# Kernel optimization log

Hardware: AMD Instinct MI355X
Metric: run time of the kernel (lower is better)

The kernel has to match this reference:

```python
import jax, jax.numpy as jnp
import numpy as np

N_NODES = 100000
N_EDGES = 3200000
D = 256
L = 3
BN_EPS = 1e-5


def setup_inputs() -> dict:
    key = jax.random.key(0)
    ks = jax.random.split(key, 6)
    scale = 1.0 / np.sqrt(D)
    x = jax.random.normal(ks[0], (N_NODES, D), dtype=jnp.float32)
    W = jax.random.normal(ks[1], (L, D, D), dtype=jnp.float32) * scale
    b = jnp.zeros((L, D), dtype=jnp.float32)
    Wl = jax.random.normal(ks[2], (L, D, D), dtype=jnp.float32) * scale
    bl = jnp.zeros((L, D), dtype=jnp.float32)
    gamma = jnp.ones((L, D), dtype=jnp.float32)
    beta = jnp.zeros((L, D), dtype=jnp.float32)
    src = jax.random.randint(ks[3], (N_EDGES,), 0, N_NODES, dtype=jnp.int32)
    dst = jax.random.randint(ks[4], (N_EDGES,), 0, N_NODES, dtype=jnp.int32)
    return {"x": x, "W": W, "b": b, "Wl": Wl, "bl": bl,
            "gamma": gamma, "beta": beta, "src": src, "dst": dst}


def _gcn_head(x, W, b, Wl, bl, gamma, beta, src, dst):
    n = x.shape[0]
    ones = jnp.ones((src.shape[0],), dtype=x.dtype)
    # degrees (clamped to 1, as DGL GraphConv does)
    deg_out = jnp.maximum(jax.ops.segment_sum(ones, src, num_segments=n), 1.0)
    deg_in = jnp.maximum(jax.ops.segment_sum(ones, dst, num_segments=n), 1.0)
    inv_sqrt_out = (deg_out ** -0.5)[:, None]  # [N,1]
    inv_sqrt_in = (deg_in ** -0.5)[:, None]

    h = x
    for l in range(W.shape[0]):
        # GraphConv, norm='both': D_in^{-1/2} A D_out^{-1/2} h W + b
        hs = h * inv_sqrt_out
        agg = jax.ops.segment_sum(hs[src], dst, num_segments=n)  # [N,D]
        agg = agg * inv_sqrt_in
        out = agg @ W[l] + b[l]
        # residual + optional linear on the layer input
        out = out + h + (h @ Wl[l] + bl[l])
        # BatchNorm1d over nodes (training-style batch stats, biased var)
        mean = jnp.mean(out, axis=0)
        var = jnp.var(out, axis=0)
        out = gamma[l] * (out - mean) * jax.lax.rsqrt(var + BN_EPS) + beta[l]
        # ReLU (Dropout treated as identity / eval mode)
        h = jax.nn.relu(out)
    return h


def reference(x, W, b, Wl, bl, gamma, beta, src, dst):
    return _gcn_head(x, W, b, Wl, bl, gamma, beta, src, dst)
```

## Files before the change

kernel.cpp:

```cpp
#include <hip/hip_runtime.h>

#define D 256
#define BN_EPS 1e-5f

typedef __attribute__((ext_vector_type(8))) short short8;
typedef __attribute__((ext_vector_type(4))) float f32x4;
typedef __attribute__((ext_vector_type(2))) float f32x2;

__device__ __forceinline__ float b2f(ushort u) {
    union { unsigned u; float f; } c; c.u = ((unsigned)u) << 16; return c.f;
}
__device__ __forceinline__ ushort f2b(float f) {
    union { float f; unsigned u; } c; c.f = f;
    return (ushort)((c.u + 0x7fffu + ((c.u >> 16) & 1u)) >> 16);
}

typedef __attribute__((address_space(1))) const void gv_t;
typedef __attribute__((address_space(3))) void lv_t;
__device__ __forceinline__ void gld16(const void* g, void* l) {
    __builtin_amdgcn_global_load_lds((gv_t*)g, (lv_t*)l, 16, 0, 0);
}

__device__ __forceinline__ uint2 pk_fp8x8(const float* r) {
    unsigned w0 = 0, w1 = 0;
    w0 = __builtin_amdgcn_cvt_pk_fp8_f32(r[0], r[1], w0, false);
    w0 = __builtin_amdgcn_cvt_pk_fp8_f32(r[2], r[3], w0, true);
    w1 = __builtin_amdgcn_cvt_pk_fp8_f32(r[4], r[5], w1, false);
    w1 = __builtin_amdgcn_cvt_pk_fp8_f32(r[6], r[7], w1, true);
    return make_uint2(w0, w1);
}


#define HB 64

__global__ __launch_bounds__(256) void hist_kernel(const int* __restrict__ src,
                                                   const int* __restrict__ dst,
                                                   unsigned* __restrict__ P, int E) {
    __shared__ unsigned lhist[16384];
    int combo = blockIdx.y;
    const int* arr = (combo >> 2) ? dst : src;
    unsigned base = (unsigned)(combo & 3) << 15;
    for (int j = threadIdx.x; j < 16384; j += 256) lhist[j] = 0;
    __syncthreads();
    int i0 = (blockIdx.x * 256 + threadIdx.x) * 4;
    int stride = HB * 256 * 4;
    for (int i = i0; i < E; i += stride) {
        if (i + 3 < E) {
            int4 v = *(const int4*)(arr + i);
            unsigned r0 = (unsigned)v.x - base;
            unsigned r1 = (unsigned)v.y - base;
            unsigned r2 = (unsigned)v.z - base;
            unsigned r3 = (unsigned)v.w - base;
            if (r0 < 32768u) atomicAdd(&lhist[r0 >> 1], 1u << ((r0 & 1) << 4));
            if (r1 < 32768u) atomicAdd(&lhist[r1 >> 1], 1u << ((r1 & 1) << 4));
            if (r2 < 32768u) atomicAdd(&lhist[r2 >> 1], 1u << ((r2 & 1) << 4));
            if (r3 < 32768u) atomicAdd(&lhist[r3 >> 1], 1u << ((r3 & 1) << 4));
        } else {
            for (int j = i; j < E; j++) {
                unsigned r = (unsigned)arr[j] - base;
                if (r < 32768u) atomicAdd(&lhist[r >> 1], 1u << ((r & 1) << 4));
            }
        }
    }
    __syncthreads();
    unsigned* dstp = P + ((size_t)(combo * HB + blockIdx.x) << 14);
    for (int j = threadIdx.x; j < 16384; j += 256) dstp[j] = lhist[j];
}

__global__ void histreduce_kernel(const unsigned* __restrict__ P,
                                  int* __restrict__ cntO, int* __restrict__ cntI, int N) {
    int g = blockIdx.x * 256 + threadIdx.x;
    int array = g >> 16;
    int p = g & 65535;
    int range = p >> 14;
    int j = p & 16383;
    const unsigned* Pp = P + ((size_t)((array * 4 + range) * HB) << 14) + j;
    unsigned s = 0;
#pragma unroll 8
    for (int b = 0; b < HB; b++) s += Pp[(size_t)b << 14];
    int bin = (range << 15) + 2 * j;
    int* cnt = array ? cntI : cntO;
    if (bin < N)     cnt[bin]     = (int)(s & 0xFFFFu);
    if (bin + 1 < N) cnt[bin + 1] = (int)(s >> 16);
}

__global__ void invsqrt_kernel(const int* __restrict__ cntO, const int* __restrict__ cntI,
                               float* __restrict__ invO, float* __restrict__ invOI,
                               float* __restrict__ sqrtO, int N) {
    int i = blockIdx.x * blockDim.x + threadIdx.x;
    if (i < N) {
        float dO = (float)max(cntO[i], 1);
        float io = rsqrtf(dO);
        invO[i] = io;
        sqrtO[i] = sqrtf(dO);
        invOI[i] = io * rsqrtf((float)max(cntI[i], 1));
    }
}

__global__ void scan1_kernel(const int* __restrict__ cnt, int* __restrict__ off,
                             int* __restrict__ bsum, int n) {
    __shared__ int s[256];
    int t = threadIdx.x;
    int i0 = blockIdx.x * 1024 + t * 4;
    int v0 = (i0 < n) ? ((cnt[i0] + 7) & ~7) : 0;
    int v1 = (i0 + 1 < n) ? ((cnt[i0 + 1] + 7) & ~7) : 0;
    int v2 = (i0 + 2 < n) ? ((cnt[i0 + 2] + 7) & ~7) : 0;
    int v3 = (i0 + 3 < n) ? ((cnt[i0 + 3] + 7) & ~7) : 0;
    int tsum = v0 + v1 + v2 + v3;
    s[t] = tsum;
    __syncthreads();
    for (int d = 1; d < 256; d <<= 1) {
        int x = (t >= d) ? s[t - d] : 0;
        __syncthreads();
        s[t] += x;
        __syncthreads();
    }
    int excl = s[t] - tsum;
    if (i0 < n)     off[i0]     = excl;
    if (i0 + 1 < n) off[i0 + 1] = excl + v0;
    if (i0 + 2 < n) off[i0 + 2] = excl + v0 + v1;
    if (i0 + 3 < n) off[i0 + 3] = excl + v0 + v1 + v2;
    if (t == 255) bsum[blockIdx.x] = s[255];
}

__global__ void scan2_kernel(int* __restrict__ bsum, int nb) {
    __shared__ int s[256];
    int t = threadIdx.x;
    int v = (t < nb) ? bsum[t] : 0;
    s[t] = v;
    __syncthreads();
    for (int d = 1; d < 256; d <<= 1) {
        int x = (t >= d) ? s[t - d] : 0;
        __syncthreads();
        s[t] += x;
        __syncthreads();
    }
    if (t < nb) bsum[t] = s[t] - v;
    if (t == nb - 1) bsum[1023] = s[t];
}

__global__ void scan3_kernel(int* __restrict__ off, const int* __restrict__ bsum,
                             int* __restrict__ bucketCur, int n) {
    int i = blockIdx.x * blockDim.x + threadIdx.x;
    if (i < n) {
        int v = off[i] + bsum[i >> 10];
        off[i] = v;
        if ((i & 255) == 0) bucketCur[i >> 8] = v;
    } else if (i == n) {
        off[n] = bsum[1023];
    }
}


#define NBKMAX 512

__global__ __launch_bounds__(256) void partA_kernel(const int* __restrict__ src,
                                                    const int* __restrict__ dst,
                                                    int* __restrict__ bucketCur,
                                                    unsigned* __restrict__ pairs,
                                                    int E, int NBK) {
    __shared__ int cnt[NBKMAX];
    __shared__ int base_s[NBKMAX];
    for (int j = threadIdx.x; j < NBK; j += 256) cnt[j] = 0;
    __syncthreads();
    for (int i = blockIdx.x * 256 + threadIdx.x; i < E; i += gridDim.x * 256)
        atomicAdd(&cnt[((unsigned)dst[i]) >> 8], 1);
    __syncthreads();
    for (int j = threadIdx.x; j < NBK; j += 256) {
        base_s[j] = atomicAdd(&bucketCur[j], cnt[j]);
        cnt[j] = 0;
    }
    __syncthreads();
    for (int i = blockIdx.x * 256 + threadIdx.x; i < E; i += gridDim.x * 256) {
        unsigned d = (unsigned)dst[i];
        unsigned b = d >> 8;
        int pos = base_s[b] + atomicAdd(&cnt[b], 1);
        pairs[pos] = ((unsigned)src[i] << 8) | (d & 255u);
    }
}

#define BCAP 14336

__global__ __launch_bounds__(256) void partB_kernel(const unsigned* __restrict__ pairs,
                                                    const int* __restrict__ off,
                                                    const int* __restrict__ bucketCur,
                                                    int* __restrict__ srcS, int N) {
    __shared__ int curL[256];
    __shared__ int stage[BCAP];
    int b = blockIdx.x;
    int n0 = b << 8;
    int n1 = min(n0 + 256, N);
    int base = off[n0];
    int len = off[n1] - base;
    if (len > BCAP) len = BCAP;
    for (int j = threadIdx.x; j < len; j += 256) stage[j] = N;
    int nn = n1 - n0;
    for (int i = threadIdx.x; i < nn; i += 256) curL[i] = off[n0 + i] - base;
    __syncthreads();
    int cntB = bucketCur[b] - base;
    for (int j = threadIdx.x; j < cntB; j += 256) {
        unsigned p = pairs[base + j];
        int pos = atomicAdd(&curL[p & 255u], 1);
        if (pos < BCAP) stage[pos] = (int)(p >> 8);
    }
    __syncthreads();
    for (int j4 = threadIdx.x; j4 * 4 < len; j4 += 256)
        *(int4*)(srcS + base + j4 * 4) = *(const int4*)(stage + j4 * 4);
}

__global__ void init_pad_kernel(ushort* __restrict__ X, unsigned* __restrict__ X8,
                                int N, long strideH) {
    int t = threadIdx.x;
    X[(size_t)N * D + t] = 0;
    if (t < 64) X8[(t >> 5) * strideH + (size_t)N * 32 + (t & 31)] = 0;
}


__global__ void prep_w_kernel(const float* __restrict__ W, const float* __restrict__ Wl,
                              const float* __restrict__ b, const float* __restrict__ bl,
                              ushort* __restrict__ Wt, float* __restrict__ bcat, int L) {
    int idx = blockIdx.x * blockDim.x + threadIdx.x;
    int k = idx & 511;
    int n = (idx >> 9) & 255;
    int l = idx >> 17;
    if (l >= L) return;
    float v;
    if (k < 256) {
        v = W[(size_t)l * 65536 + k * 256 + n];
    } else {
        v = Wl[(size_t)l * 65536 + (k - 256) * 256 + n];
        if (k - 256 == n) v += 1.0f;
    }
    Wt[idx] = f2b(v);
    if (k == 0) bcat[l * 256 + n] = b[l * 256 + n] + bl[l * 256 + n];
}

__global__ void x2b_kernel(const float* __restrict__ x, const float* __restrict__ invO,
                           ushort* __restrict__ hs, unsigned* __restrict__ hs8,
                           long strideH, long n8) {
    long i8 = (long)blockIdx.x * blockDim.x + threadIdx.x;
    if (i8 >= n8) return;
    long row = i8 >> 5;
    float sc = invO[row];
    float4 a = ((const float4*)x)[i8 * 2];
    float4 b = ((const float4*)x)[i8 * 2 + 1];
    float r[8] = { a.x * sc, a.y * sc, a.z * sc, a.w * sc,
                   b.x * sc, b.y * sc, b.z * sc, b.w * sc };
    ushort v[8];
#pragma unroll
    for (int j = 0; j < 8; j++) v[j] = f2b(r[j]);
    *(short8*)(hs + i8 * 8) = *(short8*)v;
    long H = (i8 >> 4) & 1;
    *(uint2*)(hs8 + H * strideH + row * 32 + (i8 & 15) * 2) = pk_fp8x8(r);
}


__global__ void aggregate_kernel(const unsigned* __restrict__ X8,
                                 const float* __restrict__ invOI,
                                 const int* __restrict__ off, const int* __restrict__ srcS,
                                 ushort* __restrict__ aggs, long strideH, int N) {
    const unsigned* hs8h = X8 + blockIdx.y * strideH;
    ushort* aggsh = aggs + blockIdx.y * 128;
    int tid = threadIdx.x;
    int wid = tid >> 6, lane = tid & 63;
    int l32 = lane & 31;
    int node = blockIdx.x * 8 + wid * 2 + (lane >> 5);
    if (blockIdx.x * 8 + wid * 2 >= N) return;
    bool valid = node < N;
    int e0 = valid ? off[node] : 0;
    int e1 = valid ? off[node + 1] : 0;
    f32x2 A01 = {0.f, 0.f}, A23 = {0.f, 0.f};
    for (int e = e0; e < e1; e += 8) {
        int4 c0 = *(const int4*)(srcS + e);
        int4 c1 = *(const int4*)(srcS + e + 4);
        unsigned g0 = hs8h[(size_t)c0.x * 32 + l32];
        unsigned g1 = hs8h[(size_t)c0.y * 32 + l32];
        unsigned g2 = hs8h[(size_t)c0.z * 32 + l32];
        unsigned g3 = hs8h[(size_t)c0.w * 32 + l32];
        unsigned g4 = hs8h[(size_t)c1.x * 32 + l32];
        unsigned g5 = hs8h[(size_t)c1.y * 32 + l32];
        unsigned g6 = hs8h[(size_t)c1.z * 32 + l32];
        unsigned g7 = hs8h[(size_t)c1.w * 32 + l32];
#pragma unroll
        for (int q = 0; q < 8; q++) {
            unsigned g = (q == 0) ? g0 : (q == 1) ? g1 : (q == 2) ? g2 : (q == 3) ? g3
                       : (q == 4) ? g4 : (q == 5) ? g5 : (q == 6) ? g6 : g7;
            A01 += __builtin_amdgcn_cvt_pk_f32_fp8(g, false);
            A23 += __builtin_amdgcn_cvt_pk_f32_fp8(g, true);
        }
    }
    if (valid) {
        float wi = invOI[node];
        ushort4 o;
        o.x = f2b(A01[0] * wi); o.y = f2b(A01[1] * wi);
        o.z = f2b(A23[0] * wi); o.w = f2b(A23[1] * wi);
        *(ushort4*)(aggsh + (size_t)node * D + l32 * 4) = o;
    }
}


#define BSOFF 4096

__global__ __launch_bounds__(512, 4) void gemm_kernel(
        const ushort* __restrict__ aggs, const ushort* __restrict__ hs,
        const ushort* __restrict__ Wt,  const float* __restrict__ bcat,
        const float* __restrict__ sqrtO,
        ushort* __restrict__ tmp, float* __restrict__ bnsum, float* __restrict__ bnsq,
        int M) {
    __shared__ short SH[12288];

    int bm0 = blockIdx.x * 128;
    if (bm0 >= M) return;

    int tid = threadIdx.x;
    int wid = tid >> 6, lane = tid & 63;
    int wr = wid >> 2, wc = wid & 3;
    int lrow = lane & 15, lkh = lane >> 4;
    int srow = lane >> 2;
    int sseg = (lane & 3) ^ ((srow >> 1) & 3);

    f32x4 acc[4][4] = {};

#pragma unroll
    for (int k0 = 0; k0 < 512; k0 += 32) {
        {
            int kk_ = k0 & 255;
            const ushort* Ah_ = (k0 < 256) ? aggs : hs;
            gld16(Ah_ + (size_t)(bm0 + wid * 16 + srow) * 256 + kk_ + sseg * 8,
                  SH + (wid * 16) * 32);
            const ushort* gb_ = Wt + (size_t)(wid * 32 + srow) * 512 + k0 + sseg * 8;
            gld16(gb_,            SH + BSOFF + (wid * 32) * 32);
            gld16(gb_ + 16 * 512, SH + BSOFF + (wid * 32 + 16) * 32);
        }
        __syncthreads();

        short8 a[4], bfr[4];
#pragma unroll
        for (int m = 0; m < 4; m++) {
            int ra = wr * 64 + m * 16 + lrow;
            a[m] = *(short8*)&SH[ra * 32 + (lkh ^ ((ra >> 1) & 3)) * 8];
        }
#pragma unroll
        for (int n = 0; n < 4; n++) {
            int rb = wc * 64 + n * 16 + lrow;
            bfr[n] = *(short8*)&SH[BSOFF + rb * 32 + (lkh ^ ((rb >> 1) & 3)) * 8];
        }
#pragma unroll
        for (int m = 0; m < 4; m++)
#pragma unroll
            for (int n = 0; n < 4; n++)
                acc[m][n] = __builtin_amdgcn_mfma_f32_16x16x32_bf16(a[m], bfr[n], acc[m][n], 0, 0, 0);
        __syncthreads();
    }

    ushort outv[4][4][4];
#pragma unroll
    for (int n = 0; n < 4; n++) {
        int col = wc * 64 + n * 16 + lrow;
        float bc = bcat[col];
        float s_part = 0.f, q_part = 0.f;
#pragma unroll
        for (int m = 0; m < 4; m++) {
            int rbase = bm0 + wr * 64 + m * 16 + lkh * 4;
#pragma unroll
            for (int i = 0; i < 4; i++) {
                int row = rbase + i;
                float v = (row < M) ? (acc[m][n][i] * sqrtO[row] + bc) : 0.f;
                outv[m][n][i] = f2b(v);
                if (row < M) { s_part += v; q_part += v * v; }
            }
        }
        s_part += __shfl_xor(s_part, 16);
        s_part += __shfl_xor(s_part, 32);
        q_part += __shfl_xor(q_part, 16);
        q_part += __shfl_xor(q_part, 32);
        if (lkh == 0) {
            atomicAdd(&bnsum[col], s_part);
            atomicAdd(&bnsq[col], q_part);
        }
    }

#pragma unroll
    for (int q = 0; q < 4; q++) {
        __syncthreads();
        if (wr == (q >> 1)) {
#pragma unroll
            for (int mm = 0; mm < 2; mm++) {
                int m = (q & 1) * 2 + mm;
#pragma unroll
                for (int n = 0; n < 4; n++)
#pragma unroll
                    for (int i = 0; i < 4; i++)
                        SH[(mm * 16 + lkh * 4 + i) * 256 + wc * 64 + n * 16 + lrow] =
                            (short)outv[m][n][i];
            }
        }
        __syncthreads();
        int rl = tid >> 4;
        int c0 = (tid & 15) * 16;
        int row = bm0 + q * 32 + rl;
        if (row < M) {
            *(short8*)(tmp + (size_t)row * 256 + c0)     = *(short8*)&SH[rl * 256 + c0];
            *(short8*)(tmp + (size_t)row * 256 + c0 + 8) = *(short8*)&SH[rl * 256 + c0 + 8];
        }
    }
}


__global__ void bnfin_kernel(float* __restrict__ bnsum, float* __restrict__ bnsq,
                             const float* __restrict__ gamma, const float* __restrict__ beta,
                             float2* __restrict__ bnab, float invM) {
    int c = threadIdx.x;
    float mean = bnsum[c] * invM;
    float var = bnsq[c] * invM - mean * mean;
    float a = gamma[c] * rsqrtf(var + BN_EPS);
    bnab[c] = make_float2(a, beta[c] - a * mean);
    bnsum[c] = 0.f;
    bnsq[c] = 0.f;
}

__global__ void bnrelu_kernel(const ushort* __restrict__ tmp, const float2* __restrict__ bnab,
                              const float* __restrict__ invO, ushort* __restrict__ Xout,
                              unsigned* __restrict__ X8out, long strideH,
                              float* __restrict__ out, int M, int last) {
    long i8 = (long)blockIdx.x * blockDim.x + threadIdx.x;
    if (i8 >= (long)M * 32) return;
    long row = i8 >> 5;
    int c0 = ((int)(i8 & 31)) * 8;
    short8 v = *(const short8*)(tmp + row * D + c0);
    float r[8];
#pragma unroll
    for (int j = 0; j < 8; j++) {
        float2 ab = bnab[c0 + j];
        float x = b2f((ushort)v[j]);
        r[j] = fmaxf(ab.x * x + ab.y, 0.f);
    }
    if (last) {
        float4 f0 = make_float4(r[0], r[1], r[2], r[3]);
        float4 f1 = make_float4(r[4], r[5], r[6], r[7]);
        ((float4*)(out + row * D + c0))[0] = f0;
        ((float4*)(out + row * D + c0))[1] = f1;
    } else {
        float sc = invO[row];
        ushort w[8];
#pragma unroll
        for (int j = 0; j < 8; j++) { r[j] *= sc; w[j] = f2b(r[j]); }
        *(short8*)(Xout + row * D + c0) = *(short8*)w;
        long H = (i8 >> 4) & 1;
        *(uint2*)(X8out + H * strideH + row * 32 + (i8 & 15) * 2) = pk_fp8x8(r);
    }
}


extern "C" void kernel_launch(void* const* d_in, const int* in_sizes, int n_in,
                              void* d_out, int out_size, void* d_ws, size_t ws_size,
                              hipStream_t stream) {
    const float* x     = (const float*)d_in[0];
    const float* W     = (const float*)d_in[1];
    const float* b     = (const float*)d_in[2];
    const float* Wl    = (const float*)d_in[3];
    const float* bl    = (const float*)d_in[4];
    const float* gamma = (const float*)d_in[5];
    const float* beta  = (const float*)d_in[6];
    const int*   src   = (const int*)d_in[7];
    const int*   dst   = (const int*)d_in[8];

    const int N = in_sizes[0] / D;
    const int E = in_sizes[7];
    const int L = in_sizes[1] / (D * D);
    const int M_pad = (N + 1 + 127) & ~127;
    const int E_pad = E + 7 * N + 64;
    const int NBK = (N + 255) >> 8;
    const long strideH = (long)M_pad * 32;
    float* out = (float*)d_out;

    char* p = (char*)d_ws;
    auto alloc = [&](size_t bytes) -> char* {
        char* r = p;
        p += (bytes + 255) & ~(size_t)255;
        return r;
    };
    int*      cur   = (int*)alloc((size_t)NBKMAX * 4);
    int*      cntO  = (int*)alloc((size_t)N * 4);
    int*      cntI  = (int*)alloc((size_t)N * 4);
    float*    invO  = (float*)alloc((size_t)(N + 1) * 4);
    float*    invOI = (float*)alloc((size_t)(N + 1) * 4);
    float*    sqrtO = (float*)alloc((size_t)(N + 1) * 4);
    int*      off_  = (int*)alloc((size_t)(N + 1) * 4);
    int*      bsum  = (int*)alloc(1024 * 4);
    int*      srcS  = (int*)alloc((size_t)E_pad * 4);
    ushort*   Wt    = (ushort*)alloc((size_t)L * 256 * 512 * 2);
    float*    bcat  = (float*)alloc((size_t)L * 256 * 4);
    ushort*   X     = (ushort*)alloc((size_t)M_pad * D * 2);
    unsigned* X8    = (unsigned*)alloc((size_t)2 * strideH * 4);
    ushort*   aggs  = (ushort*)alloc((size_t)M_pad * D * 2);
    ushort*   tmp   = (ushort*)alloc((size_t)M_pad * D * 2);
    float*    bnsum = (float*)alloc((size_t)2 * D * 4);
    float*    bnsq  = bnsum + D;
    float2*   bnab  = (float2*)alloc((size_t)D * 8);

    unsigned* P     = (unsigned*)aggs;
    unsigned* pairs = (unsigned*)aggs;

    {
        dim3 hg(HB, 8);
        hist_kernel<<<hg, 256, 0, stream>>>(src, dst, P, E);
        histreduce_kernel<<<512, 256, 0, stream>>>(P, cntO, cntI, N);
    }
    invsqrt_kernel<<<(N + 255) / 256, 256, 0, stream>>>(cntO, cntI, invO, invOI, sqrtO, N);
    int NB = (N + 1023) / 1024;
    scan1_kernel<<<NB, 256, 0, stream>>>(cntI, off_, bsum, N);
    scan2_kernel<<<1, 256, 0, stream>>>(bsum, NB);
    scan3_kernel<<<(N + 256) / 256, 256, 0, stream>>>(off_, bsum, cur, N);
    partA_kernel<<<512, 256, 0, stream>>>(src, dst, cur, pairs, E, NBK);
    partB_kernel<<<NBK, 256, 0, stream>>>(pairs, off_, cur, srcS, N);
    init_pad_kernel<<<1, 256, 0, stream>>>(X, X8, N, strideH);

    prep_w_kernel<<<(L * 256 * 512 + 255) / 256, 256, 0, stream>>>(W, Wl, b, bl, Wt, bcat, L);
    x2b_kernel<<<(int)(((long)N * 32 + 255) / 256), 256, 0, stream>>>(
        x, invO, X, X8, strideH, (long)N * 32);
    hipMemsetAsync(bnsum, 0, 2 * D * sizeof(float), stream);

    const int MB = (N + 127) / 128;
    const dim3 ag((N + 7) / 8, 2);
    const float invM = 1.0f / (float)N;
    for (int l = 0; l < L; l++) {
        int last = (l == L - 1);

        aggregate_kernel<<<ag, 256, 0, stream>>>(X8, invOI, off_, srcS, aggs, strideH, N);

        gemm_kernel<<<MB, 512, 0, stream>>>(aggs, X, Wt + (size_t)l * 256 * 512,
                                            bcat + l * 256, sqrtO, tmp, bnsum, bnsq, N);

        bnfin_kernel<<<1, 256, 0, stream>>>(bnsum, bnsq, gamma + l * D, beta + l * D, bnab, invM);
        bnrelu_kernel<<<(int)(((long)N * 32 + 255) / 256), 256, 0, stream>>>(
            tmp, bnab, invO, X, X8, strideH, out, N, last);
    }
}
```

Baseline: 759.1 us.

## Fuse neighbor aggregation into GEMM kernel, keeping aggregated rows in LDS

Merges the separate aggregate and GEMM kernels into one kernel. Each 64-row block gathers FP8 neighbor features into swizzled LDS, then runs the bf16 MFMA GEMM directly from LDS. This removes the global write and read of the aggregated bf16 matrix and one launch per layer. The FP8 feature layout changes from two half-width planes to one contiguous 256-byte row per node, so a full wave gathers a whole row at once. In exchange, the GEMM tile shrinks from 128 to 64 rows, which means the weight tile is reloaded more often. The gather is also serialized per wave over 8 rows, so latency hiding now depends on occupancy.

```diff
diff --git a/kernel.cpp b/kernel.cpp
--- a/kernel.cpp
+++ b/kernel.cpp
@@ -4,6 +4,7 @@
 #define BN_EPS 1e-5f
 
 typedef __attribute__((ext_vector_type(8))) short short8;
+typedef __attribute__((ext_vector_type(4))) short short4v;
 typedef __attribute__((ext_vector_type(4))) float f32x4;
 typedef __attribute__((ext_vector_type(2))) float f32x2;
 
@@ -208,11 +209,10 @@
         *(int4*)(srcS + base + j4 * 4) = *(const int4*)(stage + j4 * 4);
 }
 
-__global__ void init_pad_kernel(ushort* __restrict__ X, unsigned* __restrict__ X8,
-                                int N, long strideH) {
+__global__ void init_pad_kernel(ushort* __restrict__ X, unsigned* __restrict__ X8, int N) {
     int t = threadIdx.x;
     X[(size_t)N * D + t] = 0;
-    if (t < 64) X8[(t >> 5) * strideH + (size_t)N * 32 + (t & 31)] = 0;
+    if (t < 64) X8[(size_t)N * 64 + t] = 0;
 }
 
 
@@ -236,8 +236,7 @@
 }
 
 __global__ void x2b_kernel(const float* __restrict__ x, const float* __restrict__ invO,
-                           ushort* __restrict__ hs, unsigned* __restrict__ hs8,
-                           long strideH, long n8) {
+                           ushort* __restrict__ hs, unsigned* __restrict__ hs8, long n8) {
     long i8 = (long)blockIdx.x * blockDim.x + threadIdx.x;
     if (i8 >= n8) return;
     long row = i8 >> 5;
@@ -250,118 +249,121 @@
 #pragma unroll
     for (int j = 0; j < 8; j++) v[j] = f2b(r[j]);
     *(short8*)(hs + i8 * 8) = *(short8*)v;
-    long H = (i8 >> 4) & 1;
-    *(uint2*)(hs8 + H * strideH + row * 32 + (i8 & 15) * 2) = pk_fp8x8(r);
-}
-
-
-__global__ void aggregate_kernel(const unsigned* __restrict__ X8,
-                                 const float* __restrict__ invOI,
-                                 const int* __restrict__ off, const int* __restrict__ srcS,
-                                 ushort* __restrict__ aggs, long strideH, int N) {
-    const unsigned* hs8h = X8 + blockIdx.y * strideH;
-    ushort* aggsh = aggs + blockIdx.y * 128;
+    *(uint2*)(hs8 + i8 * 2) = pk_fp8x8(r);
+}
+
+
+#define ASTG 0
+#define BST  16384
+#define AHS  24576
+
+__global__ __launch_bounds__(512, 6) void aggemm_kernel(
+        const unsigned* __restrict__ X8, const ushort* __restrict__ hs,
+        const float* __restrict__ invOI, const float* __restrict__ sqrtO,
+        const int* __restrict__ off, const int* __restrict__ srcS,
+        const ushort* __restrict__ Wt, const float* __restrict__ bcat,
+        ushort* __restrict__ tmp, float* __restrict__ bnsum, float* __restrict__ bnsq,
+        int M) {
+    __shared__ short SH[26624];
+
+    int bm0 = blockIdx.x * 64;
     int tid = threadIdx.x;
     int wid = tid >> 6, lane = tid & 63;
-    int l32 = lane & 31;
-    int node = blockIdx.x * 8 + wid * 2 + (lane >> 5);
-    if (blockIdx.x * 8 + wid * 2 >= N) return;
-    bool valid = node < N;
-    int e0 = valid ? off[node] : 0;
-    int e1 = valid ? off[node + 1] : 0;
-    f32x2 A01 = {0.f, 0.f}, A23 = {0.f, 0.f};
-    for (int e = e0; e < e1; e += 8) {
-        int4 c0 = *(const int4*)(srcS + e);
-        int4 c1 = *(const int4*)(srcS + e + 4);
-        unsigned g0 = hs8h[(size_t)c0.x * 32 + l32];
-        unsigned g1 = hs8h[(size_t)c0.y * 32 + l32];
-        unsigned g2 = hs8h[(size_t)c0.z * 32 + l32];
-        unsigned g3 = hs8h[(size_t)c0.w * 32 + l32];
-        unsigned g4 = hs8h[(size_t)c1.x * 32 + l32];
-        unsigned g5 = hs8h[(size_t)c1.y * 32 + l32];
-        unsigned g6 = hs8h[(size_t)c1.z * 32 + l32];
-        unsigned g7 = hs8h[(size_t)c1.w * 32 + l32];
-#pragma unroll
-        for (int q = 0; q < 8; q++) {
-            unsigned g = (q == 0) ? g0 : (q == 1) ? g1 : (q == 2) ? g2 : (q == 3) ? g3
-                       : (q == 4) ? g4 : (q == 5) ? g5 : (q == 6) ? g6 : g7;
-            A01 += __builtin_amdgcn_cvt_pk_f32_fp8(g, false);
-            A23 += __builtin_amdgcn_cvt_pk_f32_fp8(g, true);
-        }
-    }
-    if (valid) {
-        float wi = invOI[node];
-        ushort4 o;
-        o.x = f2b(A01[0] * wi); o.y = f2b(A01[1] * wi);
-        o.z = f2b(A23[0] * wi); o.w = f2b(A23[1] * wi);
-        *(ushort4*)(aggsh + (size_t)node * D + l32 * 4) = o;
-    }
-}
-
-
-#define BSOFF 4096
-
-__global__ __launch_bounds__(512, 4) void gemm_kernel(
-        const ushort* __restrict__ aggs, const ushort* __restrict__ hs,
-        const ushort* __restrict__ Wt,  const float* __restrict__ bcat,
-        const float* __restrict__ sqrtO,
-        ushort* __restrict__ tmp, float* __restrict__ bnsum, float* __restrict__ bnsq,
-        int M) {
-    __shared__ short SH[12288];
-
-    int bm0 = blockIdx.x * 128;
-    if (bm0 >= M) return;
-
-    int tid = threadIdx.x;
-    int wid = tid >> 6, lane = tid & 63;
+
+    for (int r = 0; r < 8; r++) {
+        int rr = wid * 8 + r;
+        int node = bm0 + rr;
+        f32x2 A01 = {0.f, 0.f}, A23 = {0.f, 0.f};
+        float wi = 0.f;
+        if (node < M) {
+            int e0 = off[node], e1 = off[node + 1];
+            for (int e = e0; e < e1; e += 8) {
+                int4 c0 = *(const int4*)(srcS + e);
+                int4 c1 = *(const int4*)(srcS + e + 4);
+                unsigned g0 = X8[(size_t)c0.x * 64 + lane];
+                unsigned g1 = X8[(size_t)c0.y * 64 + lane];
+                unsigned g2 = X8[(size_t)c0.z * 64 + lane];
+                unsigned g3 = X8[(size_t)c0.w * 64 + lane];
+                unsigned g4 = X8[(size_t)c1.x * 64 + lane];
+                unsigned g5 = X8[(size_t)c1.y * 64 + lane];
+                unsigned g6 = X8[(size_t)c1.z * 64 + lane];
+                unsigned g7 = X8[(size_t)c1.w * 64 + lane];
+#pragma unroll
+                for (int q = 0; q < 8; q++) {
+                    unsigned g = (q == 0) ? g0 : (q == 1) ? g1 : (q == 2) ? g2 : (q == 3) ? g3
+                               : (q == 4) ? g4 : (q == 5) ? g5 : (q == 6) ? g6 : g7;
+                    A01 += __builtin_amdgcn_cvt_pk_f32_fp8(g, false);
+                    A23 += __builtin_amdgcn_cvt_pk_f32_fp8(g, true);
+                }
+            }
+            wi = invOI[node];
+        }
+        ushort o[4] = { f2b(A01[0] * wi), f2b(A01[1] * wi),
+                        f2b(A23[0] * wi), f2b(A23[1] * wi) };
+        unsigned byteoff = (unsigned)(rr * 512 + lane * 8) ^ ((unsigned)(rr & 7) << 4);
+        *(short4v*)((char*)SH + byteoff) = *(short4v*)o;
+    }
+    __syncthreads();
+
     int wr = wid >> 2, wc = wid & 3;
     int lrow = lane & 15, lkh = lane >> 4;
     int srow = lane >> 2;
     int sseg = (lane & 3) ^ ((srow >> 1) & 3);
 
-    f32x4 acc[4][4] = {};
+    f32x4 acc[2][4] = {};
 
 #pragma unroll
     for (int k0 = 0; k0 < 512; k0 += 32) {
         {
-            int kk_ = k0 & 255;
-            const ushort* Ah_ = (k0 < 256) ? aggs : hs;
-            gld16(Ah_ + (size_t)(bm0 + wid * 16 + srow) * 256 + kk_ + sseg * 8,
-                  SH + (wid * 16) * 32);
-            const ushort* gb_ = Wt + (size_t)(wid * 32 + srow) * 512 + k0 + sseg * 8;
-            gld16(gb_,            SH + BSOFF + (wid * 32) * 32);
-            gld16(gb_ + 16 * 512, SH + BSOFF + (wid * 32 + 16) * 32);
+            const ushort* gb = Wt + (size_t)(wid * 32 + srow) * 512 + k0 + sseg * 8;
+            gld16(gb,            SH + BST + (wid * 32) * 32);
+            gld16(gb + 16 * 512, SH + BST + (wid * 32 + 16) * 32);
+            if (k0 >= 256 && wid < 4) {
+                const ushort* ga = hs + (size_t)(bm0 + wid * 16 + srow) * 256
+                                   + (k0 - 256) + sseg * 8;
+                gld16(ga, SH + AHS + (wid * 16) * 32);
+            }
         }
         __syncthreads();
 
-        short8 a[4], bfr[4];
-#pragma unroll
-        for (int m = 0; m < 4; m++) {
-            int ra = wr * 64 + m * 16 + lrow;
-            a[m] = *(short8*)&SH[ra * 32 + (lkh ^ ((ra >> 1) & 3)) * 8];
+        short8 a[2], bfr[4];
+        if (k0 < 256) {
+#pragma unroll
+            for (int m = 0; m < 2; m++) {
+                int ra = wr * 32 + m * 16 + lrow;
+                unsigned bo = (unsigned)(ra * 512 + k0 * 2 + lkh * 16)
+                              ^ ((unsigned)(ra & 7) << 4);
+                a[m] = *(short8*)((char*)SH + bo);
+            }
+        } else {
+#pragma unroll
+            for (int m = 0; m < 2; m++) {
+                int ra = wr * 32 + m * 16 + lrow;
+                a[m] = *(short8*)&SH[AHS + ra * 32 + (lkh ^ ((ra >> 1) & 3)) * 8];
+            }
         }
 #pragma unroll
         for (int n = 0; n < 4; n++) {
             int rb = wc * 64 + n * 16 + lrow;
-            bfr[n] = *(short8*)&SH[BSOFF + rb * 32 + (lkh ^ ((rb >> 1) & 3)) * 8];
-        }
-#pragma unroll
-        for (int m = 0; m < 4; m++)
+            bfr[n] = *(short8*)&SH[BST + rb * 32 + (lkh ^ ((rb >> 1) & 3)) * 8];
+        }
+#pragma unroll
+        for (int m = 0; m < 2; m++)
 #pragma unroll
             for (int n = 0; n < 4; n++)
                 acc[m][n] = __builtin_amdgcn_mfma_f32_16x16x32_bf16(a[m], bfr[n], acc[m][n], 0, 0, 0);
         __syncthreads();
     }
 
-    ushort outv[4][4][4];
+    ushort outv[2][4][4];
 #pragma unroll
     for (int n = 0; n < 4; n++) {
         int col = wc * 64 + n * 16 + lrow;
         float bc = bcat[col];
         float s_part = 0.f, q_part = 0.f;
 #pragma unroll
-        for (int m = 0; m < 4; m++) {
-            int rbase = bm0 + wr * 64 + m * 16 + lkh * 4;
+        for (int m = 0; m < 2; m++) {
+            int rbase = bm0 + wr * 32 + m * 16 + lkh * 4;
 #pragma unroll
             for (int i = 0; i < 4; i++) {
                 int row = rbase + i;
@@ -380,25 +382,21 @@
         }
     }
 
-#pragma unroll
-    for (int q = 0; q < 4; q++) {
-        __syncthreads();
-        if (wr == (q >> 1)) {
-#pragma unroll
-            for (int mm = 0; mm < 2; mm++) {
-                int m = (q & 1) * 2 + mm;
-#pragma unroll
-                for (int n = 0; n < 4; n++)
-#pragma unroll
-                    for (int i = 0; i < 4; i++)
-                        SH[(mm * 16 + lkh * 4 + i) * 256 + wc * 64 + n * 16 + lrow] =
-                            (short)outv[m][n][i];
-            }
-        }
-        __syncthreads();
-        int rl = tid >> 4;
+    __syncthreads();
+#pragma unroll
+    for (int m = 0; m < 2; m++)
+#pragma unroll
+        for (int n = 0; n < 4; n++)
+#pragma unroll
+            for (int i = 0; i < 4; i++)
+                SH[(wr * 32 + m * 16 + lkh * 4 + i) * 256 + wc * 64 + n * 16 + lrow] =
+                    (short)outv[m][n][i];
+    __syncthreads();
+#pragma unroll
+    for (int p = 0; p < 2; p++) {
+        int rl = p * 32 + (tid >> 4);
         int c0 = (tid & 15) * 16;
-        int row = bm0 + q * 32 + rl;
+        int row = bm0 + rl;
         if (row < M) {
             *(short8*)(tmp + (size_t)row * 256 + c0)     = *(short8*)&SH[rl * 256 + c0];
             *(short8*)(tmp + (size_t)row * 256 + c0 + 8) = *(short8*)&SH[rl * 256 + c0 + 8];
@@ -421,8 +419,8 @@
 
 __global__ void bnrelu_kernel(const ushort* __restrict__ tmp, const float2* __restrict__ bnab,
                               const float* __restrict__ invO, ushort* __restrict__ Xout,
-                              unsigned* __restrict__ X8out, long strideH,
-                              float* __restrict__ out, int M, int last) {
+                              unsigned* __restrict__ X8out, float* __restrict__ out,
+                              int M, int last) {
     long i8 = (long)blockIdx.x * blockDim.x + threadIdx.x;
     if (i8 >= (long)M * 32) return;
     long row = i8 >> 5;
@@ -446,8 +444,7 @@
 #pragma unroll
         for (int j = 0; j < 8; j++) { r[j] *= sc; w[j] = f2b(r[j]); }
         *(short8*)(Xout + row * D + c0) = *(short8*)w;
-        long H = (i8 >> 4) & 1;
-        *(uint2*)(X8out + H * strideH + row * 32 + (i8 & 15) * 2) = pk_fp8x8(r);
+        *(uint2*)(X8out + i8 * 2) = pk_fp8x8(r);
     }
 }
 
@@ -471,7 +468,6 @@
     const int M_pad = (N + 1 + 127) & ~127;
     const int E_pad = E + 7 * N + 64;
     const int NBK = (N + 255) >> 8;
-    const long strideH = (long)M_pad * 32;
     float* out = (float*)d_out;
 
     char* p = (char*)d_ws;
@@ -492,15 +488,14 @@
     ushort*   Wt    = (ushort*)alloc((size_t)L * 256 * 512 * 2);
     float*    bcat  = (float*)alloc((size_t)L * 256 * 4);
     ushort*   X     = (ushort*)alloc((size_t)M_pad * D * 2);
-    unsigned* X8    = (unsigned*)alloc((size_t)2 * strideH * 4);
-    ushort*   aggs  = (ushort*)alloc((size_t)M_pad * D * 2);
+    unsigned* X8    = (unsigned*)alloc((size_t)M_pad * 64 * 4);
     ushort*   tmp   = (ushort*)alloc((size_t)M_pad * D * 2);
     float*    bnsum = (float*)alloc((size_t)2 * D * 4);
     float*    bnsq  = bnsum + D;
     float2*   bnab  = (float2*)alloc((size_t)D * 8);
 
-    unsigned* P     = (unsigned*)aggs;
-    unsigned* pairs = (unsigned*)aggs;
+    unsigned* P     = (unsigned*)tmp;
+    unsigned* pairs = (unsigned*)tmp;
 
     {
         dim3 hg(HB, 8);
@@ -514,26 +509,23 @@
     scan3_kernel<<<(N + 256) / 256, 256, 0, stream>>>(off_, bsum, cur, N);
     partA_kernel<<<512, 256, 0, stream>>>(src, dst, cur, pairs, E, NBK);
     partB_kernel<<<NBK, 256, 0, stream>>>(pairs, off_, cur, srcS, N);
-    init_pad_kernel<<<1, 256, 0, stream>>>(X, X8, N, strideH);
+    init_pad_kernel<<<1, 256, 0, stream>>>(X, X8, N);
 
     prep_w_kernel<<<(L * 256 * 512 + 255) / 256, 256, 0, stream>>>(W, Wl, b, bl, Wt, bcat, L);
-    x2b_kernel<<<(int)(((long)N * 32 + 255) / 256), 256, 0, stream>>>(
-        x, invO, X, X8, strideH, (long)N * 32);
+    x2b_kernel<<<(int)(((long)N * 32 + 255) / 256), 256, 0, stream>>>(x, invO, X, X8, (long)N * 32);
     hipMemsetAsync(bnsum, 0, 2 * D * sizeof(float), stream);
 
-    const int MB = (N + 127) / 128;
-    const dim3 ag((N + 7) / 8, 2);
+    const int MB64 = (N + 63) / 64;
     const float invM = 1.0f / (float)N;
     for (int l = 0; l < L; l++) {
         int last = (l == L - 1);
 
-        aggregate_kernel<<<ag, 256, 0, stream>>>(X8, invOI, off_, srcS, aggs, strideH, N);
-
-        gemm_kernel<<<MB, 512, 0, stream>>>(aggs, X, Wt + (size_t)l * 256 * 512,
-                                            bcat + l * 256, sqrtO, tmp, bnsum, bnsq, N);
+        aggemm_kernel<<<MB64, 512, 0, stream>>>(X8, X, invOI, sqrtO, off_, srcS,
+                                                Wt + (size_t)l * 256 * 512, bcat + l * 256,
+                                                tmp, bnsum, bnsq, N);
 
         bnfin_kernel<<<1, 256, 0, stream>>>(bnsum, bnsq, gamma + l * D, beta + l * D, bnab, invM);
         bnrelu_kernel<<<(int)(((long)N * 32 + 255) / 256), 256, 0, stream>>>(
-            tmp, bnab, invO, X, X8, strideH, out, N, last);
-    }
-}
+            tmp, bnab, invO, X, X8, out, N, last);
+    }
+}
```

New measurement: 870.9 us. +14.7%, slower.
